# Kernel tuning notes

Measured on AMD Instinct MI355X. Metric: run time of the kernel, lower is better.

The kernel has to match this reference:

```python
import jax, jax.numpy as jnp
import numpy as np

H = 2048      # hidden
QL = 768      # q lora rank
KVL = 512     # kv lora rank
DR = 64       # rope dim
DN = 128      # nope head dim
NH = 16       # attention heads
NIH = 8       # indexer heads
IDX = 128     # indexer key dim
BS = 16       # batch
BLK = 128     # cache block size
BPS = 32      # blocks per sequence
NB = BS * BPS # total cache blocks
MAXKV = BPS * BLK  # 4096 kv slots per seq
TOPK = 1024   # sparse attention budget


def rmsnorm(v, g, eps=1e-6):
    return v * jax.lax.rsqrt(jnp.mean(v * v, -1, keepdims=True) + eps) * g


def layernorm(v, g, b, eps=1e-6):
    c = v - jnp.mean(v, -1, keepdims=True)
    return c * jax.lax.rsqrt(jnp.mean(c * c, -1, keepdims=True) + eps) * g + b


def rope(v, sin, cos):
    h = v.shape[-1] // 2
    rot = jnp.concatenate([-v[..., h:], v[..., :h]], -1)
    return v * cos + rot * sin


def setup_inputs() -> dict:
    key = jax.random.key(0)
    ks = jax.random.split(key, 16)
    s = 0.02  # weight init scale
    ang = jax.random.uniform(ks[5], (BS, 1, DR)) * 6.2831853
    return dict(
        x=jax.random.normal(ks[0], (BS, 1, H)),
        w_dq=jax.random.normal(ks[1], (H, QL)) * s,
        w_uq_qr=jax.random.normal(ks[2], (QL, NH * (DN + DR))) * s,
        w_uk=jax.random.normal(ks[3], (NH, DN, KVL)) * s,
        w_dkv_kr=jax.random.normal(ks[4], (H, KVL + DR)) * s,
        gamma_cq=jnp.ones((QL,)),
        gamma_ckv=jnp.ones((KVL,)),
        sin=jnp.sin(ang),
        cos=jnp.cos(ang),
        cache_index=jnp.arange(BS, dtype=jnp.int32) * MAXKV,
        kv_cache=jax.random.normal(ks[6], (NB, BLK, KVL)),
        kr_cache=jax.random.normal(ks[7], (NB, BLK, DR)),
        block_table=jnp.arange(BS * BPS, dtype=jnp.int32).reshape(BS, BPS),
        act_seqs=jnp.full((BS,), MAXKV, dtype=jnp.int32),
        w_idx_qb=jax.random.normal(ks[8], (QL, NIH * IDX)) * s,
        w_idx_k=jax.random.normal(ks[9], (H, IDX)) * s,
        w_idx_proj=jax.random.normal(ks[10], (QL, NIH)) * s,
        in_gamma_k=jnp.ones((IDX,)),
        in_beta_k=jnp.zeros((IDX,)),
        index_k_cache=jax.random.normal(ks[11], (NB, BLK, IDX)),
    )


def reference(x, w_dq, w_uq_qr, w_uk, w_dkv_kr, gamma_cq, gamma_ckv, sin, cos,
              cache_index, kv_cache, kr_cache, block_table, act_seqs,
              w_idx_qb, w_idx_k, w_idx_proj, in_gamma_k, in_beta_k, index_k_cache):
    bs = x.shape[0]
    xq = x[:, 0]                      # [bs, H] (decode, q_len=1)
    s0, c0 = sin[:, 0], cos[:, 0]     # [bs, DR]

    # --- low-rank Q path ---
    cq = rmsnorm(xq @ w_dq, gamma_cq)                           # [bs, QL]
    q = (cq @ w_uq_qr).reshape(bs, NH, DN + DR)
    q_nope, q_pe = q[..., :DN], q[..., DN:]
    q_pe = rope(q_pe, s0[:, None, :], c0[:, None, :])           # [bs, NH, DR]

    # --- latent KV path + cache write ---
    ckv_kr = xq @ w_dkv_kr
    ckv = rmsnorm(ckv_kr[:, :KVL], gamma_ckv)                   # [bs, KVL]
    kr = rope(ckv_kr[:, KVL:], s0, c0)                          # [bs, DR]
    kv_flat = kv_cache.reshape(NB * BLK, KVL).at[cache_index].set(ckv)
    kr_flat = kr_cache.reshape(NB * BLK, DR).at[cache_index].set(kr)

    # --- lightning indexer ---
    ki = layernorm(xq @ w_idx_k, in_gamma_k, in_beta_k)         # [bs, IDX]
    ik_flat = index_k_cache.reshape(NB * BLK, IDX).at[cache_index].set(ki)
    qi = (cq @ w_idx_qb).reshape(bs, NIH, IDX)
    head_w = cq @ w_idx_proj                                    # [bs, NIH]

    # paged gather: flat slot ids per sequence position
    pos = (block_table * BLK)[:, :, None] + jnp.arange(BLK, dtype=block_table.dtype)
    pos = pos.reshape(bs, MAXKV)                                # [bs, MAXKV]
    ki_all = ik_flat[pos]                                       # [bs, MAXKV, IDX]

    isc = jax.nn.relu(jnp.einsum('bhd,bnd->bhn', qi, ki_all))
    isc = jnp.einsum('bh,bhn->bn', head_w, isc) / jnp.sqrt(jnp.float32(IDX))
    mask = jnp.arange(MAXKV)[None, :] < act_seqs[:, None]
    isc = jnp.where(mask, isc, -1e9)
    top_s, top_i = jax.lax.top_k(isc, TOPK)                     # [bs, TOPK]

    sel = jnp.take_along_axis(pos, top_i, axis=1)               # [bs, TOPK]
    ckv_sel = kv_flat[sel]                                      # [bs, TOPK, KVL]
    kr_sel = kr_flat[sel]                                       # [bs, TOPK, DR]

    # --- absorbed MLA attention over selected tokens ---
    q_lat = jnp.einsum('bhd,hdc->bhc', q_nope, w_uk)            # [bs, NH, KVL]
    scale = 1.0 / np.sqrt(DN + DR)
    att = (jnp.einsum('bhc,bnc->bhn', q_lat, ckv_sel)
           + jnp.einsum('bhr,bnr->bhn', q_pe, kr_sel)) * scale
    att = jnp.where((top_s > -1e8)[:, None, :], att, -1e9)
    p = jax.nn.softmax(att, axis=-1)                            # [bs, NH, TOPK]
    o_lat = jnp.einsum('bhn,bnc->bhc', p, ckv_sel)              # [bs, NH, KVL]
    o = jnp.einsum('bhc,hdc->bhd', o_lat, w_uk)                 # [bs, NH, DN]
    return o.reshape(bs, 1, NH * DN)
```

## Files before the change

kernel.cpp:

```cpp
#include <hip/hip_runtime.h>

typedef unsigned int u32;

#define BS    16
#define HDIM  2048
#define QL    768
#define KVL   512
#define DR    64
#define DN    128
#define NH    16
#define NIH   8
#define IDXD  128
#define BLK   128
#define BPS   32
#define MAXKV 4096
#define TOPK  1024
#define NCH   32

__global__ void k_dproj(const float* __restrict__ x, const float* __restrict__ w_dq,
                        const float* __restrict__ w_dkv, const float* __restrict__ w_ik,
                        float* __restrict__ dpart){
  int tile = blockIdx.x, ks = blockIdx.y, t = threadIdx.x;
  __shared__ float xs[16*128];
  __shared__ float sred[8*32*17];
  int k0 = ks*128;
  for (int idx=t; idx<16*128; idx+=256){
    int bb=idx>>7, kk=idx&127;
    xs[idx] = x[bb*HDIM + k0 + kk];
  }
  const float* wp; int ld, c0, gbase;
  if (tile < 24){ wp=w_dq;  ld=768; c0=tile*32;      gbase=0; }
  else if (tile < 42){ wp=w_dkv; ld=576; c0=(tile-24)*32; gbase=768; }
  else { wp=w_ik;  ld=128; c0=(tile-42)*32; gbase=1344; }
  int cl = t&31, kg = t>>5;
  int col = c0 + cl;
  __syncthreads();
  float acc[16];
  #pragma unroll
  for (int bb=0;bb<16;bb++) acc[bb]=0.f;
  const float* wb = wp + (size_t)(k0 + kg*16)*ld + col;
  #pragma unroll 4
  for (int kk=0; kk<16; kk++){
    float wv = wb[(size_t)kk*ld];
    int kx = kg*16+kk;
    #pragma unroll
    for (int bb=0; bb<16; bb++) acc[bb] += xs[bb*128+kx]*wv;
  }
  #pragma unroll
  for (int bb=0;bb<16;bb++) sred[(kg*32+cl)*17+bb] = acc[bb];
  __syncthreads();
  for (int r=0; r<2; r++){
    int o = r*256 + t;
    int bb = o>>5, cl2 = o&31;
    float s=0.f;
    #pragma unroll
    for (int kg2=0; kg2<8; kg2++) s += sred[(kg2*32+cl2)*17+bb];
    dpart[((size_t)ks*16 + bb)*1472 + gbase + c0 + cl2] = s;
  }
}

__global__ void k_dfin(const float* __restrict__ dpart, const float* __restrict__ g_cq,
                       const float* __restrict__ g_ckv, const float* __restrict__ sinp,
                       const float* __restrict__ cosp, const float* __restrict__ g_ik,
                       const float* __restrict__ b_ik,
                       float* __restrict__ cq, float* __restrict__ newkv,
                       float* __restrict__ newkr, float* __restrict__ newik){
  int b = blockIdx.x, sec = blockIdx.y, t = threadIdx.x;
  __shared__ float val[768];
  __shared__ float red[256];
  if (sec==0){
    for (int c=t; c<768; c+=256){
      float s = 0.f;
      for (int ks2=0; ks2<16; ks2++) s += dpart[((size_t)ks2*16+b)*1472 + c];
      val[c] = s;
    }
    __syncthreads();
    float c0v = val[t], c1v = val[t+256], c2v = val[t+512];
    red[t] = c0v*c0v + c1v*c1v + c2v*c2v;
    __syncthreads();
    for (int s=128;s>0;s>>=1){ if(t<s) red[t]+=red[t+s]; __syncthreads(); }
    float scq = 1.0f/sqrtf(red[0]/(float)QL + 1e-6f);
    cq[b*QL+t]     = c0v*scq*g_cq[t];
    cq[b*QL+t+256] = c1v*scq*g_cq[t+256];
    cq[b*QL+t+512] = c2v*scq*g_cq[t+512];
  } else if (sec==1){
    for (int c=t; c<576; c+=256){
      float s = 0.f;
      for (int ks2=0; ks2<16; ks2++) s += dpart[((size_t)ks2*16+b)*1472 + 768 + c];
      val[c] = s;
    }
    __syncthreads();
    float v0 = val[t], v1 = val[t+256];
    red[t] = v0*v0 + v1*v1;
    __syncthreads();
    for (int s=128;s>0;s>>=1){ if(t<s) red[t]+=red[t+s]; __syncthreads(); }
    float sckv = 1.0f/sqrtf(red[0]/(float)KVL + 1e-6f);
    newkv[(size_t)b*KVL + t]     = v0*sckv*g_ckv[t];
    newkv[(size_t)b*KVL + t+256] = v1*sckv*g_ckv[t+256];
    if (t<DR){
      float v = val[512+t];
      float rot = (t<32)? -val[512+t+32] : val[512+t-32];
      newkr[(size_t)b*DR + t] = v*cosp[b*DR+t] + rot*sinp[b*DR+t];
    }
  } else {
    for (int c=t; c<128; c+=256){
      float s = 0.f;
      for (int ks2=0; ks2<16; ks2++) s += dpart[((size_t)ks2*16+b)*1472 + 1344 + c];
      val[c] = s;
    }
    __syncthreads();
    red[t] = (t<128)? val[t] : 0.f;
    __syncthreads();
    for (int s=128;s>0;s>>=1){ if(t<s) red[t]+=red[t+s]; __syncthreads(); }
    float mean = red[0]/(float)IDXD;
    __syncthreads();
    float cc = (t<128)? (val[t]-mean) : 0.f;
    red[t] = cc*cc;
    __syncthreads();
    for (int s=128;s>0;s>>=1){ if(t<s) red[t]+=red[t+s]; __syncthreads(); }
    float var = red[0]/(float)IDXD;
    if (t<IDXD){
      newik[(size_t)b*IDXD + t] = cc/sqrtf(var+1e-6f)*g_ik[t] + b_ik[t];
    }
  }
}

__global__ void k_qall(const float* __restrict__ cq, const float* __restrict__ w_uq,
                       const float* __restrict__ w_qb, const float* __restrict__ w_pj,
                       float* __restrict__ qpart){
  int tile = blockIdx.x, ks = blockIdx.y, t = threadIdx.x;
  __shared__ float xs[16*192];
  __shared__ float sred[8*32*17];
  int k0 = ks*192;
  for (int idx=t; idx<16*192; idx+=256){
    int bb = idx/192, kk = idx - bb*192;
    xs[idx] = cq[bb*QL + k0 + kk];
  }
  const float* wp; int ld, c0, gbase, kind;
  if (tile < 96){ wp=w_uq; ld=3072; c0=tile*32; gbase=0; kind=0; }
  else if (tile < 128){ wp=w_qb; ld=1024; c0=(tile-96)*32; gbase=3072; kind=0; }
  else { wp=w_pj; ld=8; c0=0; gbase=4096; kind=1; }
  int cl = t&31, kg = t>>5;
  int col = c0 + cl;
  bool act = !(kind==1 && cl>=8);
  __syncthreads();
  float acc[16];
  #pragma unroll
  for (int bb=0;bb<16;bb++) acc[bb]=0.f;
  const float* wb = wp + (size_t)(k0 + kg*24)*ld + col;
  if (act){
    #pragma unroll 4
    for (int kk=0; kk<24; kk++){
      float wv = wb[(size_t)kk*ld];
      int kx = kg*24+kk;
      #pragma unroll
      for (int bb=0; bb<16; bb++) acc[bb] += xs[bb*192+kx]*wv;
    }
  }
  #pragma unroll
  for (int bb=0;bb<16;bb++) sred[(kg*32+cl)*17+bb] = acc[bb];
  __syncthreads();
  for (int r=0; r<2; r++){
    int o = r*256 + t;
    int bb = o>>5, cl2 = o&31;
    float s=0.f;
    #pragma unroll
    for (int kg2=0; kg2<8; kg2++) s += sred[(kg2*32+cl2)*17+bb];
    qpart[((size_t)ks*16 + bb)*4128 + gbase + c0 + cl2] = s;
  }
}

__global__ void k_qfin(const float* __restrict__ qpart, const float* __restrict__ sinp,
                       const float* __restrict__ cosp, float* __restrict__ qn,
                       float* __restrict__ qp, float* __restrict__ qi,
                       float* __restrict__ hw){
  int b=blockIdx.x, part=blockIdx.y, t=threadIdx.x;
  if (part<16){
    __shared__ float val[192];
    int h=part;
    if (t<192){
      int c = h*192 + t;
      float s=0.f;
      for (int ks=0; ks<4; ks++) s += qpart[((size_t)ks*16+b)*4128 + c];
      val[t]=s;
    }
    __syncthreads();
    if (t<192){
      int j=t;
      if (j<128) qn[(b*NH+h)*DN+j] = val[j];
      else {
        int d=j-128;
        float v=val[j];
        float rot = (d<32)? -val[160+d] : val[96+d];
        qp[(b*NH+h)*DR+d] = v*cosp[b*DR+d] + rot*sinp[b*DR+d];
      }
    }
  } else {
    for (int idx=t; idx<1032; idx+=256){
      int c = 3072+idx;
      float s=0.f;
      for (int ks=0; ks<4; ks++) s += qpart[((size_t)ks*16+b)*4128 + c];
      if (idx<1024) qi[b*1024 + idx] = s;
      else hw[b*NIH + idx-1024] = s;
    }
  }
}

__global__ void k_qlat(const float* __restrict__ qn, const float* __restrict__ wuk,
                       float* __restrict__ ql){
  int h=blockIdx.x, ct=blockIdx.y, t=threadIdx.x;
  __shared__ float qs[16*128];
  __shared__ float sred[4*64*17];
  for (int idx=t; idx<2048; idx+=256)
    qs[idx] = qn[((idx>>7)*NH+h)*DN + (idx&127)];
  int cl=t&63, kg=t>>6;
  int col=ct*64+cl;
  __syncthreads();
  float acc[16];
  #pragma unroll
  for (int bb=0;bb<16;bb++) acc[bb]=0.f;
  const float* wb = wuk + ((size_t)h*DN + kg*32)*KVL + col;
  #pragma unroll 4
  for (int kk=0;kk<32;kk++){
    float wv = wb[(size_t)kk*KVL];
    int kx = kg*32+kk;
    #pragma unroll
    for (int bb=0;bb<16;bb++) acc[bb]+=qs[bb*128+kx]*wv;
  }
  #pragma unroll
  for (int bb=0;bb<16;bb++) sred[(kg*64+cl)*17+bb]=acc[bb];
  __syncthreads();
  for (int r=0;r<4;r++){
    int o=r*256+t;
    int bb=o>>6, cl2=o&63;
    float s=0.f;
    #pragma unroll
    for (int kg2=0;kg2<4;kg2++) s+=sred[(kg2*64+cl2)*17+bb];
    ql[((size_t)bb*NH+h)*KVL + ct*64+cl2] = s;
  }
}

__global__ void k_isc(const float* __restrict__ qi, const float* __restrict__ hw,
                      const float* __restrict__ ikc, const int* __restrict__ btab,
                      const int* __restrict__ aseq, const int* __restrict__ cidx,
                      const float* __restrict__ newik, float* __restrict__ isc){
  int b=blockIdx.x, jb=blockIdx.y, t=threadIdx.x;
  __shared__ float K[64*132];
  __shared__ float qs[NIH*132];
  __shared__ float hs[NIH];
  __shared__ float red[64*4];
  int blk = btab[b*BPS+jb];
  int ci  = cidx[b];
  for (int idx=t; idx<NIH*IDXD; idx+=256){ int h2=idx>>7, d=idx&127; qs[h2*132+d]=qi[b*1024+idx]; }
  if (t<NIH) hs[t]=hw[b*NIH+t];
  const float4* k4   = (const float4*)(ikc + (size_t)blk*BLK*IDXD);
  const float4* nik4 = (const float4*)(newik + (size_t)b*IDXD);
  int as = aseq[b];
  int r = t>>2, hp = t&3;
  for (int half=0; half<2; half++){
    __syncthreads();
    for (int it=0; it<8; it++){
      int idx = it*256 + t;
      int rr = idx>>5, c4 = idx&31;
      int grow = blk*BLK + half*64 + rr;
      float4 v = (grow==ci)? nik4[c4] : k4[(half*64+rr)*32 + c4];
      ((float4*)&K[rr*132])[c4] = v;
    }
    __syncthreads();
    float s0=0.f, s1=0.f;
    const float4* Kr = (const float4*)&K[r*132];
    const float4* q0 = (const float4*)&qs[hp*132];
    const float4* q1 = (const float4*)&qs[(hp+4)*132];
    for (int d=0; d<32; d++){
      float4 kv=Kr[d], a=q0[d], c=q1[d];
      s0 += a.x*kv.x; s1 += c.x*kv.x;
      s0 += a.y*kv.y; s1 += c.y*kv.y;
      s0 += a.z*kv.z; s1 += c.z*kv.z;
      s0 += a.w*kv.w; s1 += c.w*kv.w;
    }
    red[r*4+hp] = hs[hp]*fmaxf(s0,0.f) + hs[hp+4]*fmaxf(s1,0.f);
    __syncthreads();
    if (t<64){
      float sc = (red[t*4]+red[t*4+1]+red[t*4+2]+red[t*4+3]) * 0.08838834764831845f;
      int n = jb*BLK + half*64 + t;
      if (n >= as) sc = -1e9f;
      isc[b*MAXKV + n] = sc;
    }
  }
}

__global__ __launch_bounds__(1024)
void k_topk(const float* __restrict__ isc, const int* __restrict__ btab,
            int* __restrict__ selp, float* __restrict__ sels){
  int b=blockIdx.x, t=threadIdx.x;
  int lane = t&63, wv = t>>6;
  __shared__ u32 su[MAXKV];
  __shared__ u32 hist[16*256];
  __shared__ u32 cum[256];
  __shared__ u32 wtot[16];
  __shared__ u32 sh_b;
  int hc = (t&15)*256;
  for (int j=0;j<4;j++){
    int i=j*1024+t;
    u32 bits=__float_as_uint(isc[b*MAXKV+i]);
    su[i] = (bits & 0x80000000u) ? ~bits : (bits | 0x80000000u);
  }
  u32 prefix=0u, need=1024u;
  for (int shift=24; shift>=0; shift-=8){
    for (int j=t;j<16*256;j+=1024) hist[j]=0u;
    __syncthreads();
    u32 hm = (shift==24)? 0u : (0xFFFFFFFFu << (shift+8));
    for (int j=0;j<4;j++){
      u32 u = su[j*1024+t];
      if ((u & hm) == prefix) atomicAdd(&hist[hc + ((u>>shift)&255u)], 1u);
    }
    __syncthreads();
    u32 v=0u;
    if (t<256){
      #pragma unroll
      for (int cpy=0;cpy<16;cpy++) v += hist[cpy*256+t];
      for (int off=1; off<64; off<<=1){
        u32 tmp = __shfl_down(v, off);
        if (lane + off < 64) v += tmp;
      }
      if (lane==0) wtot[wv]=v;
    }
    __syncthreads();
    if (t<256){
      u32 add=0u;
      for (int w2=wv+1; w2<4; w2++) add += wtot[w2];
      v += add;
      cum[t]=v;
    }
    __syncthreads();
    if (t<256){
      u32 nxt = (t<255)? cum[t+1] : 0u;
      if (v>=need && nxt<need) sh_b = (u32)t;
    }
    __syncthreads();
    u32 B = sh_b;
    u32 aboveB = (B<255u)? cum[B+1] : 0u;
    need -= aboveB;
    prefix |= (B<<shift);
    __syncthreads();
  }
  u32 T = prefix;
  u32 cG=0u,cE=0u;
  for (int j=0;j<4;j++){ u32 u=su[j*1024+t]; cG += (u>T)?1u:0u; cE += (u==T)?1u:0u; }
  u32 packed = (cG<<16) | cE;
  u32 v = packed;
  for (int off=1; off<64; off<<=1){
    u32 tmp = __shfl_up(v, off);
    if (lane >= off) v += tmp;
  }
  if (lane==63) wtot[wv]=v;
  __syncthreads();
  u32 add=0u;
  for (int w2=0; w2<wv; w2++) add += wtot[w2];
  u32 excl = v + add - packed;
  u32 total = 0u;
  #pragma unroll
  for (int w2=0; w2<16; w2++) total += wtot[w2];
  u32 mGT = total>>16;
  u32 keepEq = 1024u - mGT;
  u32 gG = excl>>16, gE = excl&0xFFFFu;
  for (int j=0;j<4;j++){
    int i=j*1024+t; u32 u=su[i];
    int slot=-1;
    if (u>T) slot=(int)(gG++);
    else if (u==T){ u32 r2=gE++; if (r2<keepEq) slot=(int)(mGT+r2); }
    if (slot>=0){
      int pos = btab[b*BPS + (i>>7)]*BLK + (i&127);
      selp[b*TOPK+slot]=pos;
      sels[b*TOPK+slot]=isc[b*MAXKV+i];
    }
  }
}

__global__ __launch_bounds__(256, 2)
void k_fgat(const float* __restrict__ qlat, const float* __restrict__ qpe,
            const float* __restrict__ kvc, const float* __restrict__ krc,
            const int* __restrict__ selp, const float* __restrict__ sels,
            const int* __restrict__ cidx, const float* __restrict__ newkv,
            const float* __restrict__ newkr,
            float* __restrict__ opart, float* __restrict__ mch,
            float* __restrict__ lch){
  int ch=blockIdx.x, b=blockIdx.y, t=threadIdx.x;
  __shared__ float K[32*580];
  __shared__ float sP[32*16];
  int lane31 = t&31;
  int sp_l   = selp[b*TOPK + ch*32 + lane31];
  float sv_l = sels[b*TOPK + ch*32 + lane31];
  int ci = cidx[b];
  const float4* kv4  = (const float4*)kvc;
  const float4* kr4  = (const float4*)krc;
  const float4* nkv4 = (const float4*)newkv;
  const float4* nkr4 = (const float4*)newkr;
  float4 rA[18];
  #pragma unroll
  for (int j=0;j<18;j++){
    int idx=j*256+t, r=idx/144, c=idx-r*144;
    int row = __shfl(sp_l, r, 64);
    const float4* src;
    if (c<128) src = (row==ci)? (nkv4 + (size_t)b*128 + c) : (kv4 + (size_t)row*128 + c);
    else       src = (row==ci)? (nkr4 + (size_t)b*16 + (c-128)) : (kr4 + (size_t)row*16 + (c-128));
    rA[j] = *src;
  }
  int hp = t>>5, sub = (t>>4)&1, kc = t&15;
  const float4* qlA = (const float4*)(qlat + ((size_t)b*NH+hp)*KVL);
  const float4* qpA = (const float4*)(qpe  + ((size_t)b*NH+hp)*DR);
  const float4* qlB = (const float4*)(qlat + ((size_t)b*NH+hp+8)*KVL);
  const float4* qpB = (const float4*)(qpe  + ((size_t)b*NH+hp+8)*DR);
  float4 qa[9], qb[9];
  #pragma unroll
  for (int j=0;j<9;j++){
    int g = kc*9 + j;
    qa[j] = (g<128)? qlA[g] : qpA[g-128];
    qb[j] = (g<128)? qlB[g] : qpB[g-128];
  }
  #pragma unroll
  for (int j=0;j<18;j++){
    int idx=j*256+t, r=idx/144, c=idx-r*144;
    ((float4*)&K[r*580])[c] = rA[j];
  }
  __syncthreads();
  const float scale = 0.07216878364870323f;
  float pa=0.f, pb=0.f;
  for (int rl=0; rl<16; rl++){
    int r = sub*16 + rl;
    const float4* Kc = (const float4*)&K[r*580 + kc*36];
    float sA=0.f, sB=0.f;
    #pragma unroll
    for (int j=0;j<9;j++){
      float4 kv=Kc[j];
      sA += kv.x*qa[j].x + kv.y*qa[j].y + kv.z*qa[j].z + kv.w*qa[j].w;
      sB += kv.x*qb[j].x + kv.y*qb[j].y + kv.z*qb[j].z + kv.w*qb[j].w;
    }
    #pragma unroll
    for (int mm=1;mm<16;mm<<=1){
      sA += __shfl_xor(sA, mm, 16);
      sB += __shfl_xor(sB, mm, 16);
    }
    float svr = __shfl(sv_l, r, 64);
    float vA = (svr > -1e8f)? sA*scale : -1e9f;
    float vB = (svr > -1e8f)? sB*scale : -1e9f;
    if (kc==rl){ pa = vA; pb = vB; }
  }
  float mA = pa, mB = pb;
  #pragma unroll
  for (int mm=1;mm<32;mm<<=1){
    mA = fmaxf(mA, __shfl_xor(mA, mm, 32));
    mB = fmaxf(mB, __shfl_xor(mB, mm, 32));
  }
  pa = expf(pa - mA); pb = expf(pb - mB);
  float lA = pa, lB = pb;
  #pragma unroll
  for (int mm=1;mm<32;mm<<=1){
    lA += __shfl_xor(lA, mm, 32);
    lB += __shfl_xor(lB, mm, 32);
  }
  int r31 = sub*16 + kc;
  sP[r31*16 + hp]     = pa;
  sP[r31*16 + hp + 8] = pb;
  if (r31==0){
    mch[(b*NCH+ch)*16 + hp]     = mA;
    mch[(b*NCH+ch)*16 + hp + 8] = mB;
    lch[(b*NCH+ch)*16 + hp]     = lA;
    lch[(b*NCH+ch)*16 + hp + 8] = lB;
  }
  __syncthreads();
  int l6 = t&63, hg = t>>6;
  const float4* sP4 = (const float4*)sP;
  float4 a0[4], a1[4];
  #pragma unroll
  for (int hq=0;hq<4;hq++){
    a0[hq].x=a0[hq].y=a0[hq].z=a0[hq].w=0.f;
    a1[hq].x=a1[hq].y=a1[hq].z=a1[hq].w=0.f;
  }
  for (int r=0;r<32;r++){
    const float4* Vr = (const float4*)&K[r*580];
    float4 v0 = Vr[l6], v1 = Vr[64+l6];
    float4 p4 = sP4[r*4 + hg];
    a0[0].x+=p4.x*v0.x; a0[0].y+=p4.x*v0.y; a0[0].z+=p4.x*v0.z; a0[0].w+=p4.x*v0.w;
    a1[0].x+=p4.x*v1.x; a1[0].y+=p4.x*v1.y; a1[0].z+=p4.x*v1.z; a1[0].w+=p4.x*v1.w;
    a0[1].x+=p4.y*v0.x; a0[1].y+=p4.y*v0.y; a0[1].z+=p4.y*v0.z; a0[1].w+=p4.y*v0.w;
    a1[1].x+=p4.y*v1.x; a1[1].y+=p4.y*v1.y; a1[1].z+=p4.y*v1.z; a1[1].w+=p4.y*v1.w;
    a0[2].x+=p4.z*v0.x; a0[2].y+=p4.z*v0.y; a0[2].z+=p4.z*v0.z; a0[2].w+=p4.z*v0.w;
    a1[2].x+=p4.z*v1.x; a1[2].y+=p4.z*v1.y; a1[2].z+=p4.z*v1.z; a1[2].w+=p4.z*v1.w;
    a0[3].x+=p4.w*v0.x; a0[3].y+=p4.w*v0.y; a0[3].z+=p4.w*v0.z; a0[3].w+=p4.w*v0.w;
    a1[3].x+=p4.w*v1.x; a1[3].y+=p4.w*v1.y; a1[3].z+=p4.w*v1.z; a1[3].w+=p4.w*v1.w;
  }
  #pragma unroll
  for (int hq=0;hq<4;hq++){
    int hh = hg*4 + hq;
    float4* dst = (float4*)(opart + (((size_t)(b*NCH+ch))*NH + hh)*KVL);
    dst[l6]    = a0[hq];
    dst[64+l6] = a1[hq];
  }
}

__global__ void k_comb(const float* __restrict__ opart, const float* __restrict__ mch,
                       const float* __restrict__ lch, const float* __restrict__ wuk,
                       float* __restrict__ out){
  int b=blockIdx.x, h=blockIdx.y, t=threadIdx.x;
  __shared__ float sOl[KVL];
  __shared__ float sCoef[NCH];
  __shared__ float sInvL;
  if (t<NCH){
    float mv = mch[(b*NCH+t)*16+h];
    float lv = lch[(b*NCH+t)*16+h];
    float M = mv;
    for (int off=1; off<NCH; off<<=1) M = fmaxf(M, __shfl_xor(M, off, NCH));
    float coef = expf(mv - M);
    float Lp = lv*coef;
    for (int off=1; off<NCH; off<<=1) Lp += __shfl_xor(Lp, off, NCH);
    sCoef[t] = coef;
    if (t==0) sInvL = 1.0f/Lp;
  }
  __syncthreads();
  for (int c=t; c<KVL; c+=128){
    float s=0.f;
    for (int ch=0; ch<NCH; ch++)
      s += opart[(((size_t)(b*NCH+ch))*NH + h)*KVL + c] * sCoef[ch];
    sOl[c] = s*sInvL;
  }
  __syncthreads();
  const float4* w4 = (const float4*)(wuk + ((size_t)(h*DN)+t)*KVL);
  const float4* o4 = (const float4*)sOl;
  float a=0.f;
  for (int v=0; v<128; v++){
    float4 w = w4[v]; float4 o = o4[v];
    a += w.x*o.x + w.y*o.y + w.z*o.z + w.w*o.w;
  }
  out[b*(NH*DN) + h*DN + t] = a;
}

extern "C" void kernel_launch(void* const* d_in, const int* in_sizes, int n_in,
                              void* d_out, int out_size, void* d_ws, size_t ws_size,
                              hipStream_t stream){
  const float* x        =(const float*)d_in[0];
  const float* w_dq     =(const float*)d_in[1];
  const float* w_uq_qr  =(const float*)d_in[2];
  const float* w_uk     =(const float*)d_in[3];
  const float* w_dkv_kr =(const float*)d_in[4];
  const float* g_cq     =(const float*)d_in[5];
  const float* g_ckv    =(const float*)d_in[6];
  const float* sinp     =(const float*)d_in[7];
  const float* cosp     =(const float*)d_in[8];
  const int*   cidx     =(const int*)d_in[9];
  const float* kvc      =(const float*)d_in[10];
  const float* krc      =(const float*)d_in[11];
  const int*   btab     =(const int*)d_in[12];
  const int*   aseq     =(const int*)d_in[13];
  const float* w_idx_qb =(const float*)d_in[14];
  const float* w_idx_k  =(const float*)d_in[15];
  const float* w_idx_pj =(const float*)d_in[16];
  const float* g_ik     =(const float*)d_in[17];
  const float* b_ik     =(const float*)d_in[18];
  const float* ikc      =(const float*)d_in[19];

  float* ws    = (float*)d_ws;
  float* cq    = ws;
  float* qnope = ws + 12288;
  float* qpe   = ws + 45056;
  float* qlat  = ws + 61440;
  float* qi    = ws + 192512;
  float* hw    = ws + 208896;
  float* isc   = ws + 209024;
  int*   selp  = (int*)(ws + 274560);
  float* sels  = ws + 290944;
  float* dpart = ws + 307328;
  float* qpart = ws + 684160;
  float* mch   = ws + 948352;
  float* lch   = ws + 956544;
  float* opart = ws + 964736;
  float* newkv = ws + 5159040;
  float* newkr = ws + 5167232;
  float* newik = ws + 5168256;

  k_dproj<<<dim3(46,16),  dim3(256),0,stream>>>(x,w_dq,w_dkv_kr,w_idx_k,dpart);
  k_dfin <<<dim3(BS,3),   dim3(256),0,stream>>>(dpart,g_cq,g_ckv,sinp,cosp,g_ik,b_ik,cq,newkv,newkr,newik);
  k_qall <<<dim3(129,4),  dim3(256),0,stream>>>(cq,w_uq_qr,w_idx_qb,w_idx_pj,qpart);
  k_qfin <<<dim3(BS,17),  dim3(256),0,stream>>>(qpart,sinp,cosp,qnope,qpe,qi,hw);
  k_qlat <<<dim3(16,8),   dim3(256),0,stream>>>(qnope,w_uk,qlat);
  k_isc  <<<dim3(BS,BPS), dim3(256),0,stream>>>(qi,hw,ikc,btab,aseq,cidx,newik,isc);
  k_topk <<<dim3(BS),     dim3(1024),0,stream>>>(isc,btab,selp,sels);
  k_fgat <<<dim3(NCH,BS), dim3(256),0,stream>>>(qlat,qpe,kvc,krc,selp,sels,cidx,newkv,newkr,opart,mch,lch);
  k_comb <<<dim3(BS,NH),  dim3(128),0,stream>>>(opart,mch,lch,w_uk,(float*)d_out);
}
```

Baseline: 331.7 us.

## Fold q split-K reduction into qlat and isc kernels, drop k_qfin

Removes the k_qfin launch: k_qlat now sums the four split-K partials itself and applies rope to produce q_pe, and k_isc sums the partials for indexer queries and head weights. k_isc loads the whole 128-row key block at once and computes two rows per thread, cutting barriers, with launch bounds requesting two blocks per CU. k_qlat is moved after top-k, and redundant partial reductions are repeated across blocks in exchange for one fewer launch and intermediate buffer.

```diff
diff --git a/kernel.cpp b/kernel.cpp
--- a/kernel.cpp
+++ b/kernel.cpp
@@ -170,52 +170,29 @@
   }
 }
 
-__global__ void k_qfin(const float* __restrict__ qpart, const float* __restrict__ sinp,
-                       const float* __restrict__ cosp, float* __restrict__ qn,
-                       float* __restrict__ qp, float* __restrict__ qi,
-                       float* __restrict__ hw){
-  int b=blockIdx.x, part=blockIdx.y, t=threadIdx.x;
-  if (part<16){
-    __shared__ float val[192];
-    int h=part;
-    if (t<192){
-      int c = h*192 + t;
-      float s=0.f;
-      for (int ks=0; ks<4; ks++) s += qpart[((size_t)ks*16+b)*4128 + c];
-      val[t]=s;
-    }
-    __syncthreads();
-    if (t<192){
-      int j=t;
-      if (j<128) qn[(b*NH+h)*DN+j] = val[j];
-      else {
-        int d=j-128;
-        float v=val[j];
-        float rot = (d<32)? -val[160+d] : val[96+d];
-        qp[(b*NH+h)*DR+d] = v*cosp[b*DR+d] + rot*sinp[b*DR+d];
-      }
-    }
-  } else {
-    for (int idx=t; idx<1032; idx+=256){
-      int c = 3072+idx;
-      float s=0.f;
-      for (int ks=0; ks<4; ks++) s += qpart[((size_t)ks*16+b)*4128 + c];
-      if (idx<1024) qi[b*1024 + idx] = s;
-      else hw[b*NIH + idx-1024] = s;
-    }
-  }
-}
-
-__global__ void k_qlat(const float* __restrict__ qn, const float* __restrict__ wuk,
-                       float* __restrict__ ql){
+__global__ void k_qlat(const float* __restrict__ qpart, const float* __restrict__ sinp,
+                       const float* __restrict__ cosp, const float* __restrict__ wuk,
+                       float* __restrict__ qp, float* __restrict__ ql){
   int h=blockIdx.x, ct=blockIdx.y, t=threadIdx.x;
-  __shared__ float qs[16*128];
+  __shared__ float qs[16*193];
   __shared__ float sred[4*64*17];
-  for (int idx=t; idx<2048; idx+=256)
-    qs[idx] = qn[((idx>>7)*NH+h)*DN + (idx&127)];
+  for (int idx=t; idx<16*192; idx+=256){
+    int bb=idx/192, cc=idx-bb*192;
+    float s=0.f;
+    for (int ks=0;ks<4;ks++) s += qpart[((size_t)ks*16+bb)*4128 + h*192 + cc];
+    qs[bb*193+cc]=s;
+  }
+  __syncthreads();
+  if (ct==0){
+    for (int idx=t; idx<1024; idx+=256){
+      int bb=idx>>6, d=idx&63;
+      float v = qs[bb*193+128+d];
+      float rot = (d<32)? -qs[bb*193+160+d] : qs[bb*193+96+d];
+      qp[(bb*NH+h)*DR+d] = v*cosp[bb*DR+d] + rot*sinp[bb*DR+d];
+    }
+  }
   int cl=t&63, kg=t>>6;
   int col=ct*64+cl;
-  __syncthreads();
   float acc[16];
   #pragma unroll
   for (int bb=0;bb<16;bb++) acc[bb]=0.f;
@@ -225,7 +202,7 @@
     float wv = wb[(size_t)kk*KVL];
     int kx = kg*32+kk;
     #pragma unroll
-    for (int bb=0;bb<16;bb++) acc[bb]+=qs[bb*128+kx]*wv;
+    for (int bb=0;bb<16;bb++) acc[bb]+=qs[bb*193+kx]*wv;
   }
   #pragma unroll
   for (int bb=0;bb<16;bb++) sred[(kg*64+cl)*17+bb]=acc[bb];
@@ -240,52 +217,61 @@
   }
 }
 
-__global__ void k_isc(const float* __restrict__ qi, const float* __restrict__ hw,
-                      const float* __restrict__ ikc, const int* __restrict__ btab,
-                      const int* __restrict__ aseq, const int* __restrict__ cidx,
-                      const float* __restrict__ newik, float* __restrict__ isc){
+__global__ __launch_bounds__(256, 2)
+void k_isc(const float* __restrict__ qpart, const float* __restrict__ ikc,
+           const int* __restrict__ btab, const int* __restrict__ aseq,
+           const int* __restrict__ cidx, const float* __restrict__ newik,
+           float* __restrict__ isc){
   int b=blockIdx.x, jb=blockIdx.y, t=threadIdx.x;
-  __shared__ float K[64*132];
+  __shared__ float K[128*132];
   __shared__ float qs[NIH*132];
   __shared__ float hs[NIH];
-  __shared__ float red[64*4];
+  __shared__ float red[128*4];
   int blk = btab[b*BPS+jb];
   int ci  = cidx[b];
-  for (int idx=t; idx<NIH*IDXD; idx+=256){ int h2=idx>>7, d=idx&127; qs[h2*132+d]=qi[b*1024+idx]; }
-  if (t<NIH) hs[t]=hw[b*NIH+t];
+  for (int idx=t; idx<NIH*IDXD; idx+=256){
+    int h2=idx>>7, d=idx&127;
+    float s=0.f;
+    for (int ks=0;ks<4;ks++) s += qpart[((size_t)ks*16+b)*4128 + 3072 + idx];
+    qs[h2*132+d]=s;
+  }
+  if (t<NIH){
+    float s=0.f;
+    for (int ks=0;ks<4;ks++) s += qpart[((size_t)ks*16+b)*4128 + 4096 + t];
+    hs[t]=s;
+  }
   const float4* k4   = (const float4*)(ikc + (size_t)blk*BLK*IDXD);
   const float4* nik4 = (const float4*)(newik + (size_t)b*IDXD);
   int as = aseq[b];
+  for (int it=0; it<16; it++){
+    int idx = it*256 + t;
+    int rr = idx>>5, c4 = idx&31;
+    int grow = blk*BLK + rr;
+    float4 v = (grow==ci)? nik4[c4] : k4[rr*32 + c4];
+    ((float4*)&K[rr*132])[c4] = v;
+  }
+  __syncthreads();
   int r = t>>2, hp = t&3;
-  for (int half=0; half<2; half++){
-    __syncthreads();
-    for (int it=0; it<8; it++){
-      int idx = it*256 + t;
-      int rr = idx>>5, c4 = idx&31;
-      int grow = blk*BLK + half*64 + rr;
-      float4 v = (grow==ci)? nik4[c4] : k4[(half*64+rr)*32 + c4];
-      ((float4*)&K[rr*132])[c4] = v;
-    }
-    __syncthreads();
-    float s0=0.f, s1=0.f;
-    const float4* Kr = (const float4*)&K[r*132];
-    const float4* q0 = (const float4*)&qs[hp*132];
-    const float4* q1 = (const float4*)&qs[(hp+4)*132];
-    for (int d=0; d<32; d++){
-      float4 kv=Kr[d], a=q0[d], c=q1[d];
-      s0 += a.x*kv.x; s1 += c.x*kv.x;
-      s0 += a.y*kv.y; s1 += c.y*kv.y;
-      s0 += a.z*kv.z; s1 += c.z*kv.z;
-      s0 += a.w*kv.w; s1 += c.w*kv.w;
-    }
-    red[r*4+hp] = hs[hp]*fmaxf(s0,0.f) + hs[hp+4]*fmaxf(s1,0.f);
-    __syncthreads();
-    if (t<64){
-      float sc = (red[t*4]+red[t*4+1]+red[t*4+2]+red[t*4+3]) * 0.08838834764831845f;
-      int n = jb*BLK + half*64 + t;
-      if (n >= as) sc = -1e9f;
-      isc[b*MAXKV + n] = sc;
-    }
+  float s00=0.f,s01=0.f,s10=0.f,s11=0.f;
+  const float4* K0 = (const float4*)&K[r*132];
+  const float4* K1 = (const float4*)&K[(r+64)*132];
+  const float4* q0 = (const float4*)&qs[hp*132];
+  const float4* q1 = (const float4*)&qs[(hp+4)*132];
+  for (int d=0; d<32; d++){
+    float4 kv0=K0[d], kv1=K1[d], a=q0[d], c=q1[d];
+    s00 += a.x*kv0.x; s01 += c.x*kv0.x; s10 += a.x*kv1.x; s11 += c.x*kv1.x;
+    s00 += a.y*kv0.y; s01 += c.y*kv0.y; s10 += a.y*kv1.y; s11 += c.y*kv1.y;
+    s00 += a.z*kv0.z; s01 += c.z*kv0.z; s10 += a.z*kv1.z; s11 += c.z*kv1.z;
+    s00 += a.w*kv0.w; s01 += c.w*kv0.w; s10 += a.w*kv1.w; s11 += c.w*kv1.w;
+  }
+  red[r*4+hp]      = hs[hp]*fmaxf(s00,0.f) + hs[hp+4]*fmaxf(s01,0.f);
+  red[(r+64)*4+hp] = hs[hp]*fmaxf(s10,0.f) + hs[hp+4]*fmaxf(s11,0.f);
+  __syncthreads();
+  if (t<128){
+    float sc = (red[t*4]+red[t*4+1]+red[t*4+2]+red[t*4+3]) * 0.08838834764831845f;
+    int n = jb*BLK + t;
+    if (n >= as) sc = -1e9f;
+    isc[b*MAXKV + n] = sc;
   }
 }
 
@@ -561,30 +547,26 @@
 
   float* ws    = (float*)d_ws;
   float* cq    = ws;
-  float* qnope = ws + 12288;
-  float* qpe   = ws + 45056;
-  float* qlat  = ws + 61440;
-  float* qi    = ws + 192512;
-  float* hw    = ws + 208896;
-  float* isc   = ws + 209024;
-  int*   selp  = (int*)(ws + 274560);
-  float* sels  = ws + 290944;
-  float* dpart = ws + 307328;
-  float* qpart = ws + 684160;
-  float* mch   = ws + 948352;
-  float* lch   = ws + 956544;
-  float* opart = ws + 964736;
-  float* newkv = ws + 5159040;
-  float* newkr = ws + 5167232;
-  float* newik = ws + 5168256;
+  float* qpe   = ws + 12288;
+  float* qlat  = ws + 28672;
+  float* isc   = ws + 159744;
+  int*   selp  = (int*)(ws + 225280);
+  float* sels  = ws + 241664;
+  float* dpart = ws + 258048;
+  float* qpart = ws + 634880;
+  float* mch   = ws + 899072;
+  float* lch   = ws + 907264;
+  float* opart = ws + 915456;
+  float* newkv = ws + 5109760;
+  float* newkr = ws + 5117952;
+  float* newik = ws + 5118976;
 
   k_dproj<<<dim3(46,16),  dim3(256),0,stream>>>(x,w_dq,w_dkv_kr,w_idx_k,dpart);
   k_dfin <<<dim3(BS,3),   dim3(256),0,stream>>>(dpart,g_cq,g_ckv,sinp,cosp,g_ik,b_ik,cq,newkv,newkr,newik);
   k_qall <<<dim3(129,4),  dim3(256),0,stream>>>(cq,w_uq_qr,w_idx_qb,w_idx_pj,qpart);
-  k_qfin <<<dim3(BS,17),  dim3(256),0,stream>>>(qpart,sinp,cosp,qnope,qpe,qi,hw);
-  k_qlat <<<dim3(16,8),   dim3(256),0,stream>>>(qnope,w_uk,qlat);
-  k_isc  <<<dim3(BS,BPS), dim3(256),0,stream>>>(qi,hw,ikc,btab,aseq,cidx,newik,isc);
+  k_isc  <<<dim3(BS,BPS), dim3(256),0,stream>>>(qpart,ikc,btab,aseq,cidx,newik,isc);
   k_topk <<<dim3(BS),     dim3(1024),0,stream>>>(isc,btab,selp,sels);
+  k_qlat <<<dim3(16,8),   dim3(256),0,stream>>>(qpart,sinp,cosp,w_uk,qpe,qlat);
   k_fgat <<<dim3(NCH,BS), dim3(256),0,stream>>>(qlat,qpe,kvc,krc,selp,sels,cidx,newkv,newkr,opart,mch,lch);
   k_comb <<<dim3(BS,NH),  dim3(128),0,stream>>>(opart,mch,lch,w_uk,(float*)d_out);
 }
```

After: 335.7 us. Within noise of the previous version (+1.2%).
